# Optimization experiments

Measured on AMD Instinct MI355X. Metric: run time of the kernel, lower is better.

## Reference

```python
import jax, jax.numpy as jnp
import numpy as np
from jax import lax

T, H, K, V, O = 8192, 2048, 512, 512, 2048


def setup_inputs() -> dict:
    key = jax.random.key(0)
    ks = jax.random.split(key, 11)
    s_h = 1.0 / np.sqrt(H)
    s_v = 1.0 / np.sqrt(V)
    return {
        "hidden_state": jax.random.normal(ks[0], (T, H), jnp.float32),
        "Wq": jax.random.normal(ks[1], (H, K), jnp.float32) * s_h,
        "bq": jax.random.normal(ks[2], (K,), jnp.float32) * 0.02,
        "Wk": jax.random.normal(ks[3], (H, K), jnp.float32) * s_h,
        "bk": jax.random.normal(ks[4], (K,), jnp.float32) * 0.02,
        "Wv": jax.random.normal(ks[5], (H, V), jnp.float32) * s_h,
        "bv": jax.random.normal(ks[6], (V,), jnp.float32) * 0.02,
        "Wg": jax.random.normal(ks[7], (H, K), jnp.float32) * s_h,
        "bg": jax.random.normal(ks[8], (K,), jnp.float32) * 0.02,
        "Wo": jax.random.normal(ks[9], (V, O), jnp.float32) * s_v,
        "bo": jax.random.normal(ks[10], (O,), jnp.float32) * 0.02,
    }


def reference(hidden_state, Wq, bq, Wk, bk, Wv, bv, Wg, bg, Wo, bo):
    # Batched projections (torch Linear: x @ W^T + b; here W stored as [in,out])
    q = hidden_state @ Wq + bq                    # [T, K]
    k = jax.nn.sigmoid(hidden_state @ Wk + bk)    # [T, K]
    g = jax.nn.sigmoid(hidden_state @ Wg + bg)    # [T, K]
    v = hidden_state @ Wv + bv                    # [T, V]

    def step(state, qkvg):
        qi, ki, vi, gi = qkvg
        # state: [K, V]; gated decay per key-dim row, then outer-product write
        state = state * gi[:, None] + ki[:, None] * vi[None, :]
        out_i = qi @ state  # == state.T @ qi -> [V]
        return state, out_i

    init = jnp.zeros((K, V), hidden_state.dtype)
    final_state, outs = lax.scan(step, init, (q, k, v, g))  # outs: [T, V]
    output = outs @ Wo + bo                                  # [T, O]
    return output, final_state
```

## Files before the change

kernel.cpp:

```cpp
#include <hip/hip_runtime.h>

#define T_LEN 8192
#define H_DIM 2048
#define K_DIM 512
#define V_DIM 512
#define O_DIM 2048
#define CHUNK 64
#define NCHUNK 128
#define CGROUP 64

typedef short bf16x8 __attribute__((ext_vector_type(8)));
typedef float f32x4 __attribute__((ext_vector_type(4)));

typedef const __attribute__((address_space(1))) void* gptr1_t;
typedef __attribute__((address_space(3))) void* lptr3_t;

__device__ __forceinline__ float b2f(unsigned short u) {
    unsigned int i = ((unsigned int)u) << 16;
    float f;
    __builtin_memcpy(&f, &i, 4);
    return f;
}
__device__ __forceinline__ unsigned short f2b(float f) {
    unsigned int i;
    __builtin_memcpy(&i, &f, 4);
    unsigned int r = (i + 0x7FFFu + ((i >> 16) & 1u)) >> 16;
    return (unsigned short)r;
}
__device__ __forceinline__ float fw(float v) {
    return fminf(fmaxf(v, -1e30f), 1e30f);
}

__global__ __launch_bounds__(256) void conv2bf_k(const float* __restrict__ in,
                                                 unsigned short* __restrict__ out,
                                                 long N) {
    long i = ((long)blockIdx.x * 256 + threadIdx.x) * 8;
    if (i >= N) return;
    unsigned int w[4];
#pragma unroll
    for (int u = 0; u < 4; u++) {
        unsigned short lo = f2b(in[i + 2 * u]);
        unsigned short hi = f2b(in[i + 2 * u + 1]);
        w[u] = (unsigned int)lo | ((unsigned int)hi << 16);
    }
    uint4 pk; pk.x = w[0]; pk.y = w[1]; pk.z = w[2]; pk.w = w[3];
    *(uint4*)(out + i) = pk;
}

__global__ __launch_bounds__(64) void probe_k(int* __restrict__ flag) {
    __shared__ unsigned short As[16 * 32];
    __shared__ unsigned short Bs[16 * 32];
    int tid = threadIdx.x;
    for (int idx = tid; idx < 512; idx += 64) {
        int r = idx >> 5, c = idx & 31;
        float av = (c == 0) ? (float)(r + 1) : (c == 1 ? 1.0f : 0.0f);
        float bv = (c == 0) ? 1.0f : (c == 1 ? (float)(1024 * (r + 1)) : 0.0f);
        As[r * 32 + c] = f2b(av);
        Bs[r * 32 + c] = f2b(bv);
    }
    __syncthreads();
    int ln15 = tid & 15, q4 = (tid & 63) >> 4;
    bf16x8 a = *(const bf16x8*)(As + ln15 * 32 + q4 * 8);
    bf16x8 b = *(const bf16x8*)(Bs + ln15 * 32 + q4 * 8);
    f32x4 acc = {0.f, 0.f, 0.f, 0.f};
    acc = __builtin_amdgcn_mfma_f32_16x16x32_bf16(a, b, acc, 0, 0, 0);
    bool h0 = true, h1 = true;
#pragma unroll
    for (int i = 0; i < 4; i++) {
        float e0 = (float)((q4 * 4 + i + 1) + 1024 * (ln15 + 1));
        float e1 = (float)((ln15 + 1) + 1024 * (q4 * 4 + i + 1));
        h0 = h0 && (acc[i] == e0);
        h1 = h1 && (acc[i] == e1);
    }
    unsigned long long b0 = __ballot(h0 ? 1 : 0);
    unsigned long long b1 = __ballot(h1 ? 1 : 0);
    if (tid == 0) *flag = (b0 == ~0ull) ? 0 : ((b1 == ~0ull) ? 1 : 0);
}

template <int DF>
__global__ __launch_bounds__(256) void transpose_k(const void* __restrict__ in,
                                                   unsigned short* __restrict__ out,
                                                   int R, int C) {
    __shared__ unsigned short tile[32][33];
    int br = blockIdx.x, bc = blockIdx.y;
    int tc = threadIdx.x & 31, tr = threadIdx.x >> 5;
#pragma unroll
    for (int i = 0; i < 4; i++) {
        int r = tr + 8 * i;
        long idx = (long)(br * 32 + r) * C + bc * 32 + tc;
        tile[r][tc] = DF ? f2b(((const float*)in)[idx]) : ((const unsigned short*)in)[idx];
    }
    __syncthreads();
#pragma unroll
    for (int i = 0; i < 4; i++) {
        int r = tr + 8 * i;
        out[(long)(bc * 32 + r) * R + br * 32 + tc] = tile[tc][r];
    }
}

__global__ __launch_bounds__(256) void proj_gemm_k(const unsigned short* __restrict__ A,
                                                   const unsigned short* __restrict__ WT,
                                                   const float* __restrict__ bq,
                                                   const float* __restrict__ bk,
                                                   const float* __restrict__ bg,
                                                   const float* __restrict__ bv,
                                                   unsigned short* __restrict__ qb,
                                                   unsigned short* __restrict__ kb,
                                                   float* __restrict__ gb,
                                                   unsigned short* __restrict__ vT,
                                                   const int* __restrict__ flagp) {
    __shared__ unsigned short As[128 * 32];
    __shared__ unsigned short Bs[128 * 32];
    int fl = *flagp;
    int tid = threadIdx.x;
    int lane = tid & 63;
    int w = tid >> 6;
    int ln15 = lane & 15, q4 = lane >> 4;
    int wm = w >> 1, wn = w & 1;
    long m0 = (long)blockIdx.x * 128, n0 = (long)blockIdx.y * 128;

    f32x4 acc[4][4] = {};

    for (int kt = 0; kt < H_DIM; kt += 32) {
        __syncthreads();
#pragma unroll
        for (int it = 0; it < 2; it++) {
            int chunk = it * 256 + tid;
            int row = chunk >> 2;
            int col = (chunk & 3) * 8;
            const unsigned short* ga = A + (m0 + row) * (long)H_DIM + kt + col;
            const unsigned short* gb_ = WT + (n0 + row) * (long)H_DIM + kt + col;
            __builtin_amdgcn_global_load_lds((gptr1_t)(const void*)ga,
                                             (lptr3_t)(void*)(As + chunk * 8), 16, 0, 0);
            __builtin_amdgcn_global_load_lds((gptr1_t)(const void*)gb_,
                                             (lptr3_t)(void*)(Bs + chunk * 8), 16, 0, 0);
        }
        __syncthreads();
        bf16x8 a[4], b[4];
#pragma unroll
        for (int i = 0; i < 4; i++)
            a[i] = *(const bf16x8*)(As + (wm * 64 + 16 * i + ln15) * 32 + q4 * 8);
#pragma unroll
        for (int j = 0; j < 4; j++)
            b[j] = *(const bf16x8*)(Bs + (wn * 64 + 16 * j + ln15) * 32 + q4 * 8);
#pragma unroll
        for (int i = 0; i < 4; i++)
#pragma unroll
            for (int j = 0; j < 4; j++)
                acc[i][j] = __builtin_amdgcn_mfma_f32_16x16x32_bf16(a[i], b[j], acc[i][j], 0, 0, 0);
    }

    int seg = (int)(n0 >> 9);
    int nl0 = (int)(n0 & 511);
    const float* bias = seg == 0 ? bq : seg == 1 ? bk : seg == 2 ? bg : bv;

    if (seg == 3 && fl == 0) {
#pragma unroll
        for (int i = 0; i < 4; i++)
#pragma unroll
            for (int j = 0; j < 4; j++) {
                int nl = nl0 + wn * 64 + 16 * j + ln15;
                float bsv = bias[nl];
                long mb = m0 + wm * 64 + 16 * i + q4 * 4;
                unsigned short h0 = f2b(fw(acc[i][j][0] + bsv));
                unsigned short h1 = f2b(fw(acc[i][j][1] + bsv));
                unsigned short h2 = f2b(fw(acc[i][j][2] + bsv));
                unsigned short h3 = f2b(fw(acc[i][j][3] + bsv));
                uint2 pk;
                pk.x = (unsigned int)h0 | ((unsigned int)h1 << 16);
                pk.y = (unsigned int)h2 | ((unsigned int)h3 << 16);
                *(uint2*)(vT + (long)nl * T_LEN + mb) = pk;
            }
    } else {
#pragma unroll
        for (int i = 0; i < 4; i++)
#pragma unroll
            for (int j = 0; j < 4; j++)
#pragma unroll
                for (int ii = 0; ii < 4; ii++) {
                    int dm = fl ? ln15 : q4 * 4 + ii;
                    int dn = fl ? q4 * 4 + ii : ln15;
                    long m = m0 + wm * 64 + 16 * i + dm;
                    int nl = nl0 + wn * 64 + 16 * j + dn;
                    float v = fw(acc[i][j][ii] + bias[nl]);
                    if (seg == 1 || seg == 2) v = 1.0f / (1.0f + __expf(-v));
                    if (seg == 0)
                        qb[m * K_DIM + nl] = f2b(v);
                    else if (seg == 1)
                        kb[m * K_DIM + nl] = f2b(v);
                    else if (seg == 2)
                        gb[m * K_DIM + nl] = v;
                    else
                        vT[(long)nl * T_LEN + m] = f2b(v);
                }
    }
}

__global__ __launch_bounds__(256) void gemm_f32_k(const unsigned short* __restrict__ A,
                                                  const unsigned short* __restrict__ BT,
                                                  const float* __restrict__ bias,
                                                  float* __restrict__ out,
                                                  int M, int N, int K,
                                                  const int* __restrict__ flagp) {
    __shared__ unsigned short As[128 * 32];
    __shared__ unsigned short Bs[128 * 32];
    int fl = *flagp;
    int tid = threadIdx.x;
    int lane = tid & 63;
    int w = tid >> 6;
    int ln15 = lane & 15, q4 = lane >> 4;
    int wm = w >> 1, wn = w & 1;
    long m0 = (long)blockIdx.x * 128, n0 = (long)blockIdx.y * 128;

    f32x4 acc[4][4] = {};

    for (int kt = 0; kt < K; kt += 32) {
        __syncthreads();
#pragma unroll
        for (int it = 0; it < 2; it++) {
            int chunk = it * 256 + tid;
            int row = chunk >> 2;
            int col = (chunk & 3) * 8;
            const unsigned short* ga = A + (m0 + row) * (long)K + kt + col;
            const unsigned short* gbp = BT + (n0 + row) * (long)K + kt + col;
            __builtin_amdgcn_global_load_lds((gptr1_t)(const void*)ga,
                                             (lptr3_t)(void*)(As + chunk * 8), 16, 0, 0);
            __builtin_amdgcn_global_load_lds((gptr1_t)(const void*)gbp,
                                             (lptr3_t)(void*)(Bs + chunk * 8), 16, 0, 0);
        }
        __syncthreads();
        bf16x8 a[4], b[4];
#pragma unroll
        for (int i = 0; i < 4; i++)
            a[i] = *(const bf16x8*)(As + (wm * 64 + 16 * i + ln15) * 32 + q4 * 8);
#pragma unroll
        for (int j = 0; j < 4; j++)
            b[j] = *(const bf16x8*)(Bs + (wn * 64 + 16 * j + ln15) * 32 + q4 * 8);
#pragma unroll
        for (int i = 0; i < 4; i++)
#pragma unroll
            for (int j = 0; j < 4; j++)
                acc[i][j] = __builtin_amdgcn_mfma_f32_16x16x32_bf16(a[i], b[j], acc[i][j], 0, 0, 0);
    }

#pragma unroll
    for (int i = 0; i < 4; i++)
#pragma unroll
        for (int j = 0; j < 4; j++)
#pragma unroll
            for (int ii = 0; ii < 4; ii++) {
                int dm = fl ? ln15 : q4 * 4 + ii;
                int dn = fl ? q4 * 4 + ii : ln15;
                long m = m0 + wm * 64 + 16 * i + dm;
                long n = n0 + wn * 64 + 16 * j + dn;
                out[m * N + n] = fw(acc[i][j][ii] + bias[n]);
            }
}

__global__ __launch_bounds__(256) void cumprod_k(const float* __restrict__ g,
                                                 unsigned short* __restrict__ q,
                                                 unsigned short* __restrict__ k,
                                                 unsigned short* __restrict__ khatT,
                                                 float* __restrict__ pend) {
    int c = blockIdx.x;
    int d = blockIdx.y * 256 + threadIdx.x;
    long base = (long)c * CHUNK * K_DIM + d;
    float P = 1.0f;
    for (int s = 0; s < CHUNK; s++) P = fmaxf(P * g[base + (long)s * K_DIM], 1e-37f);
    pend[c * K_DIM + d] = P;
    float Pend = P;
    P = 1.0f;
    for (int s8 = 0; s8 < CHUNK; s8 += 8) {
        unsigned int packed[4];
#pragma unroll
        for (int u = 0; u < 8; u++) {
            int s = s8 + u;
            long idx = base + (long)s * K_DIM;
            P = fmaxf(P * g[idx], 1e-37f);
            float qv = fw(b2f(q[idx]) * P);
            q[idx] = f2b(qv);
            float kv = b2f(k[idx]);
            float kt = kv / P;
            kt = fmaxf(fminf(kt, 3e37f), -3e37f);
            k[idx] = f2b(kt);
            float ratio = Pend / P;
            unsigned short kh = f2b(fw(kv * ratio));
            if (u & 1)
                packed[u >> 1] |= ((unsigned int)kh) << 16;
            else
                packed[u >> 1] = kh;
        }
        uint4 pk;
        pk.x = packed[0]; pk.y = packed[1]; pk.z = packed[2]; pk.w = packed[3];
        *(uint4*)(khatT + (long)d * T_LEN + c * CHUNK + s8) = pk;
    }
}

__global__ __launch_bounds__(256) void scan_k(const unsigned short* __restrict__ khatT,
                                              const unsigned short* __restrict__ vT,
                                              const float* __restrict__ pend,
                                              unsigned short* __restrict__ ST,
                                              float* __restrict__ Sio,
                                              int c0, int cn,
                                              const int* __restrict__ flagp) {
    int fl = *flagp;
    int lane = threadIdx.x & 63, w = threadIdx.x >> 6;
    int ln15 = lane & 15, q4 = lane >> 4;
    int k0 = (blockIdx.x & 15) * 32 + (w & 1) * 16;
    int v0 = (blockIdx.x >> 4) * 32 + (w >> 1) * 16;
    f32x4 acc;
#pragma unroll
    for (int i = 0; i < 4; i++) {
        int dk = fl ? ln15 : q4 * 4 + i;
        int dv = fl ? q4 * 4 + i : ln15;
        acc[i] = Sio[(long)(k0 + dk) * V_DIM + v0 + dv];
    }
    for (int c = c0; c < cn; c++) {
        long cloc = c - c0;
        if (!fl) {
            uint2 pk;
            pk.x = (unsigned int)f2b(fw(acc[0])) | ((unsigned int)f2b(fw(acc[1])) << 16);
            pk.y = (unsigned int)f2b(fw(acc[2])) | ((unsigned int)f2b(fw(acc[3])) << 16);
            *(uint2*)(ST + (cloc * V_DIM + v0 + ln15) * K_DIM + k0 + q4 * 4) = pk;
            float4 pd = *(const float4*)(pend + c * K_DIM + k0 + q4 * 4);
            acc[0] *= pd.x; acc[1] *= pd.y; acc[2] *= pd.z; acc[3] *= pd.w;
        } else {
#pragma unroll
            for (int i = 0; i < 4; i++)
                ST[(cloc * V_DIM + v0 + q4 * 4 + i) * K_DIM + k0 + ln15] = f2b(fw(acc[i]));
            float pd = pend[c * K_DIM + k0 + ln15];
#pragma unroll
            for (int i = 0; i < 4; i++) acc[i] *= pd;
        }
#pragma unroll
        for (int s0 = 0; s0 < CHUNK; s0 += 32) {
            bf16x8 a = *(const bf16x8*)(khatT + (long)(k0 + ln15) * T_LEN + c * CHUNK + s0 + q4 * 8);
            bf16x8 b = *(const bf16x8*)(vT + (long)(v0 + ln15) * T_LEN + c * CHUNK + s0 + q4 * 8);
            acc = __builtin_amdgcn_mfma_f32_16x16x32_bf16(a, b, acc, 0, 0, 0);
        }
    }
#pragma unroll
    for (int i = 0; i < 4; i++) {
        int dk = fl ? ln15 : q4 * 4 + i;
        int dv = fl ? q4 * 4 + i : ln15;
        Sio[(long)(k0 + dk) * V_DIM + v0 + dv] = fw(acc[i]);
    }
}

__global__ __launch_bounds__(256) void copy_state_k(const float* __restrict__ S,
                                                    float* __restrict__ out) {
    long i = (long)blockIdx.x * 1024 + threadIdx.x * 4;
    *(float4*)(out + i) = *(const float4*)(S + i);
}

__global__ __launch_bounds__(256) void intra_k(const unsigned short* __restrict__ qs,
                                               const unsigned short* __restrict__ ks,
                                               const unsigned short* __restrict__ vT,
                                               const unsigned short* __restrict__ ST,
                                               unsigned short* __restrict__ outs,
                                               int c_base,
                                               const int* __restrict__ flagp) {
    __shared__ unsigned short Ab[64 * 72];
    int fl = *flagp;
    long cloc = blockIdx.x >> 1;
    int c = c_base + (int)cloc, h = blockIdx.x & 1;
    int lane = threadIdx.x & 63, w = threadIdx.x >> 6;
    int ln15 = lane & 15, q4 = lane >> 4;
    long t0 = (long)c * CHUNK;

    {
        f32x4 accA[4] = {};
        for (int kk = 0; kk < K_DIM; kk += 32) {
            bf16x8 a = *(const bf16x8*)(qs + (t0 + 16 * w + ln15) * K_DIM + kk + q4 * 8);
#pragma unroll
            for (int j = 0; j < 4; j++) {
                bf16x8 b = *(const bf16x8*)(ks + (t0 + 16 * j + ln15) * K_DIM + kk + q4 * 8);
                accA[j] = __builtin_amdgcn_mfma_f32_16x16x32_bf16(a, b, accA[j], 0, 0, 0);
            }
        }
#pragma unroll
        for (int j = 0; j < 4; j++)
#pragma unroll
            for (int i = 0; i < 4; i++) {
                int dt = fl ? ln15 : q4 * 4 + i;
                int ds = fl ? q4 * 4 + i : ln15;
                int tl = 16 * w + dt;
                int s = 16 * j + ds;
                float av = (s <= tl) ? accA[j][i] : 0.0f;
                Ab[tl * 72 + s] = f2b(fw(av));
            }
    }
    __syncthreads();

    int v0 = h * 256 + w * 64;
    f32x4 acc[4][4] = {};
    for (int kk = 0; kk < K_DIM; kk += 32) {
        bf16x8 a[4], b[4];
#pragma unroll
        for (int i = 0; i < 4; i++)
            a[i] = *(const bf16x8*)(qs + (t0 + 16 * i + ln15) * K_DIM + kk + q4 * 8);
#pragma unroll
        for (int j = 0; j < 4; j++)
            b[j] = *(const bf16x8*)(ST + (cloc * V_DIM + v0 + 16 * j + ln15) * K_DIM + kk + q4 * 8);
#pragma unroll
        for (int i = 0; i < 4; i++)
#pragma unroll
            for (int j = 0; j < 4; j++)
                acc[i][j] = __builtin_amdgcn_mfma_f32_16x16x32_bf16(a[i], b[j], acc[i][j], 0, 0, 0);
    }
#pragma unroll
    for (int s0 = 0; s0 < CHUNK; s0 += 32) {
        bf16x8 a[4], b[4];
#pragma unroll
        for (int i = 0; i < 4; i++)
            a[i] = *(const bf16x8*)(Ab + (16 * i + ln15) * 72 + s0 + q4 * 8);
#pragma unroll
        for (int j = 0; j < 4; j++)
            b[j] = *(const bf16x8*)(vT + (long)(v0 + 16 * j + ln15) * T_LEN + t0 + s0 + q4 * 8);
#pragma unroll
        for (int i = 0; i < 4; i++)
#pragma unroll
            for (int j = 0; j < 4; j++)
                acc[i][j] = __builtin_amdgcn_mfma_f32_16x16x32_bf16(a[i], b[j], acc[i][j], 0, 0, 0);
    }
#pragma unroll
    for (int i = 0; i < 4; i++)
#pragma unroll
        for (int j = 0; j < 4; j++)
#pragma unroll
            for (int ii = 0; ii < 4; ii++) {
                int dt = fl ? ln15 : q4 * 4 + ii;
                int dv = fl ? q4 * 4 + ii : ln15;
                outs[(t0 + 16 * i + dt) * V_DIM + v0 + 16 * j + dv] = f2b(fw(acc[i][j][ii]));
            }
}

extern "C" void kernel_launch(void* const* d_in, const int* in_sizes, int n_in,
                              void* d_out, int out_size, void* d_ws, size_t ws_size,
                              hipStream_t stream) {
    const float* hs = (const float*)d_in[0];
    const float* Wq = (const float*)d_in[1];
    const float* bq = (const float*)d_in[2];
    const float* Wk = (const float*)d_in[3];
    const float* bk = (const float*)d_in[4];
    const float* Wv = (const float*)d_in[5];
    const float* bv = (const float*)d_in[6];
    const float* Wg = (const float*)d_in[7];
    const float* bg = (const float*)d_in[8];
    const float* Wo = (const float*)d_in[9];
    const float* bo = (const float*)d_in[10];

    float* out = (float*)d_out;

    char* ws = (char*)d_ws;
    const size_t MB = 1024 * 1024;
    unsigned short* WT = (unsigned short*)(ws + 0 * MB);
    unsigned short* WoT = (unsigned short*)(ws + 8 * MB);
    unsigned short* qb = (unsigned short*)(ws + 10 * MB);
    unsigned short* kb = (unsigned short*)(ws + 18 * MB);
    unsigned short* vTb = (unsigned short*)(ws + 26 * MB);
    float* gb = (float*)(ws + 34 * MB);
    unsigned short* outsb = (unsigned short*)(ws + 34 * MB);
    unsigned short* khatT = (unsigned short*)(ws + 50 * MB);
    float* pend = (float*)(ws + 58 * MB);
    int* flags = (int*)(ws + 58 * MB + 256 * 1024);
    float* Scarry = (float*)(ws + 59 * MB);
    unsigned short* STb = (unsigned short*)(ws + 60 * MB);
    unsigned short* hsb = (unsigned short*)(ws + 60 * MB);
    float* fsspare = (float*)(ws + 92 * MB);
    (void)ws_size; (void)in_sizes; (void)n_in;

    float* finalst =
        ((long)out_size >= (long)T_LEN * O_DIM + (long)K_DIM * V_DIM)
            ? out + (long)T_LEN * O_DIM
            : fsspare;

    dim3 b256(256);
    hipMemsetAsync(flags, 0, 16, stream);
    probe_k<<<dim3(1), dim3(64), 0, stream>>>(flags);
    conv2bf_k<<<dim3(8192), b256, 0, stream>>>(hs, hsb, (long)T_LEN * H_DIM);
    transpose_k<1><<<dim3(H_DIM / 32, K_DIM / 32), b256, 0, stream>>>(Wq, WT + 0 * 512 * H_DIM, H_DIM, K_DIM);
    transpose_k<1><<<dim3(H_DIM / 32, K_DIM / 32), b256, 0, stream>>>(Wk, WT + 1 * 512 * H_DIM, H_DIM, K_DIM);
    transpose_k<1><<<dim3(H_DIM / 32, K_DIM / 32), b256, 0, stream>>>(Wg, WT + 2 * 512 * H_DIM, H_DIM, K_DIM);
    transpose_k<1><<<dim3(H_DIM / 32, V_DIM / 32), b256, 0, stream>>>(Wv, WT + 3 * 512 * H_DIM, H_DIM, V_DIM);
    transpose_k<1><<<dim3(V_DIM / 32, O_DIM / 32), b256, 0, stream>>>(Wo, WoT, V_DIM, O_DIM);
    proj_gemm_k<<<dim3(T_LEN / 128, 16), b256, 0, stream>>>(
        hsb, WT, bq, bk, bg, bv, qb, kb, gb, vTb, flags);
    cumprod_k<<<dim3(NCHUNK, K_DIM / 256), b256, 0, stream>>>(gb, qb, kb, khatT, pend);
    hipMemsetAsync(Scarry, 0, (size_t)K_DIM * V_DIM * 4, stream);
    scan_k<<<dim3(256), b256, 0, stream>>>(khatT, vTb, pend, STb, Scarry, 0, CGROUP, flags);
    intra_k<<<dim3(2 * CGROUP), b256, 0, stream>>>(qb, kb, vTb, STb, outsb, 0, flags);
    scan_k<<<dim3(256), b256, 0, stream>>>(khatT, vTb, pend, STb, Scarry, CGROUP, NCHUNK, flags);
    intra_k<<<dim3(2 * CGROUP), b256, 0, stream>>>(qb, kb, vTb, STb, outsb, CGROUP, flags);
    copy_state_k<<<dim3((K_DIM * V_DIM) / 1024), b256, 0, stream>>>(Scarry, finalst);
    gemm_f32_k<<<dim3(T_LEN / 128, O_DIM / 128), b256, 0, stream>>>(
        outsb, WoT, bo, out, T_LEN, O_DIM, V_DIM, flags);
}
```

Before: 482.1 us.

## Rewrite projection GEMM as 256x256 tile double-buffered pipelined kernel with swizzled LDS

```diff
diff --git a/kernel.cpp b/kernel.cpp
--- a/kernel.cpp
+++ b/kernel.cpp
@@ -98,56 +98,153 @@
     }
 }
 
-__global__ __launch_bounds__(256) void proj_gemm_k(const unsigned short* __restrict__ A,
-                                                   const unsigned short* __restrict__ WT,
-                                                   const float* __restrict__ bq,
-                                                   const float* __restrict__ bk,
-                                                   const float* __restrict__ bg,
-                                                   const float* __restrict__ bv,
-                                                   unsigned short* __restrict__ qb,
-                                                   unsigned short* __restrict__ kb,
-                                                   float* __restrict__ gb,
-                                                   unsigned short* __restrict__ vT,
-                                                   const int* __restrict__ flagp) {
-    __shared__ unsigned short As[128 * 32];
-    __shared__ unsigned short Bs[128 * 32];
+__global__ __launch_bounds__(512, 2) void proj_gemm256_k(const unsigned short* __restrict__ A,
+                                                         const unsigned short* __restrict__ WT,
+                                                         const float* __restrict__ bq,
+                                                         const float* __restrict__ bk,
+                                                         const float* __restrict__ bg,
+                                                         const float* __restrict__ bv,
+                                                         unsigned short* __restrict__ qb,
+                                                         unsigned short* __restrict__ kb,
+                                                         float* __restrict__ gb,
+                                                         unsigned short* __restrict__ vT,
+                                                         const int* __restrict__ flagp) {
+    __shared__ unsigned short As[2][256 * 64];
+    __shared__ unsigned short Bs[2][256 * 64];
     int fl = *flagp;
     int tid = threadIdx.x;
     int lane = tid & 63;
+    int ln15 = lane & 15, q4 = lane >> 4;
     int w = tid >> 6;
-    int ln15 = lane & 15, q4 = lane >> 4;
-    int wm = w >> 1, wn = w & 1;
-    long m0 = (long)blockIdx.x * 128, n0 = (long)blockIdx.y * 128;
-
-    f32x4 acc[4][4] = {};
-
-    for (int kt = 0; kt < H_DIM; kt += 32) {
-        __syncthreads();
-#pragma unroll
-        for (int it = 0; it < 2; it++) {
-            int chunk = it * 256 + tid;
-            int row = chunk >> 2;
-            int col = (chunk & 3) * 8;
-            const unsigned short* ga = A + (m0 + row) * (long)H_DIM + kt + col;
-            const unsigned short* gb_ = WT + (n0 + row) * (long)H_DIM + kt + col;
-            __builtin_amdgcn_global_load_lds((gptr1_t)(const void*)ga,
-                                             (lptr3_t)(void*)(As + chunk * 8), 16, 0, 0);
-            __builtin_amdgcn_global_load_lds((gptr1_t)(const void*)gb_,
-                                             (lptr3_t)(void*)(Bs + chunk * 8), 16, 0, 0);
-        }
-        __syncthreads();
-        bf16x8 a[4], b[4];
-#pragma unroll
-        for (int i = 0; i < 4; i++)
-            a[i] = *(const bf16x8*)(As + (wm * 64 + 16 * i + ln15) * 32 + q4 * 8);
-#pragma unroll
-        for (int j = 0; j < 4; j++)
-            b[j] = *(const bf16x8*)(Bs + (wn * 64 + 16 * j + ln15) * 32 + q4 * 8);
-#pragma unroll
-        for (int i = 0; i < 4; i++)
-#pragma unroll
-            for (int j = 0; j < 4; j++)
-                acc[i][j] = __builtin_amdgcn_mfma_f32_16x16x32_bf16(a[i], b[j], acc[i][j], 0, 0, 0);
+    int wm = w >> 2, wn = w & 3;
+    long m0 = (long)blockIdx.x * 256, n0 = (long)blockIdx.y * 256;
+
+    int idx0 = tid, idx1 = 512 + tid;
+    int r0_ = idx0 >> 3, r1_ = idx1 >> 3;
+    int c80 = (idx0 & 7) ^ (r0_ & 7);
+    int c81 = (idx1 & 7) ^ (r1_ & 7);
+    int trA0 = ((r0_ >> 6) & 1) * 128 + (r0_ & 63);
+    int trA1 = ((r1_ >> 6) & 1) * 128 + (r1_ & 63);
+    int tcB0 = ((r0_ >> 5) & 3) * 64 + (r0_ & 31);
+    int tcB1 = ((r1_ >> 5) & 3) * 64 + (r1_ & 31);
+    const unsigned short* gA0 = A + (m0 + trA0) * (long)H_DIM + c80 * 8;
+    const unsigned short* gA1 = A + (m0 + trA1) * (long)H_DIM + c81 * 8;
+    const unsigned short* gB0 = WT + (n0 + tcB0) * (long)H_DIM + c80 * 8;
+    const unsigned short* gB1 = WT + (n0 + tcB1) * (long)H_DIM + c81 * 8;
+    int ld0 = idx0 * 8, ld1 = idx1 * 8;
+
+#define STAGE_A(buf, half, ks)                                                              \
+    do {                                                                                    \
+        __builtin_amdgcn_global_load_lds(                                                   \
+            (gptr1_t)(const void*)(gA0 + (long)(half) * 64 * H_DIM + (ks)),                 \
+            (lptr3_t)(void*)(&As[buf][(half) * 8192 + ld0]), 16, 0, 0);                     \
+        __builtin_amdgcn_global_load_lds(                                                   \
+            (gptr1_t)(const void*)(gA1 + (long)(half) * 64 * H_DIM + (ks)),                 \
+            (lptr3_t)(void*)(&As[buf][(half) * 8192 + ld1]), 16, 0, 0);                     \
+    } while (0)
+#define STAGE_B(buf, half, ks)                                                              \
+    do {                                                                                    \
+        __builtin_amdgcn_global_load_lds(                                                   \
+            (gptr1_t)(const void*)(gB0 + (long)(half) * 32 * H_DIM + (ks)),                 \
+            (lptr3_t)(void*)(&Bs[buf][(half) * 8192 + ld0]), 16, 0, 0);                     \
+        __builtin_amdgcn_global_load_lds(                                                   \
+            (gptr1_t)(const void*)(gB1 + (long)(half) * 32 * H_DIM + (ks)),                 \
+            (lptr3_t)(void*)(&Bs[buf][(half) * 8192 + ld1]), 16, 0, 0);                     \
+    } while (0)
+
+    auto LDA = [&](int buf, int im, int s) -> bf16x8 {
+        int row = (im >> 2) * 128 + wm * 64 + (im & 3) * 16 + ln15;
+        int cb = (s * 64 + q4 * 16) ^ ((row & 7) << 4);
+        return *(const bf16x8*)((const unsigned short*)As[buf] + row * 64 + (cb >> 1));
+    };
+    auto LDB = [&](int buf, int jn, int s) -> bf16x8 {
+        int row = (jn >> 1) * 128 + wn * 32 + (jn & 1) * 16 + ln15;
+        int cb = (s * 64 + q4 * 16) ^ ((row & 7) << 4);
+        return *(const bf16x8*)((const unsigned short*)Bs[buf] + row * 64 + (cb >> 1));
+    };
+
+    f32x4 acc[8][4] = {};
+
+    STAGE_A(0, 0, 0);
+    STAGE_B(0, 0, 0);
+    STAGE_B(0, 1, 0);
+    STAGE_A(0, 1, 0);
+    STAGE_A(1, 0, 64);
+    STAGE_B(1, 0, 64);
+    asm volatile("s_waitcnt vmcnt(4)" ::: "memory");
+    __builtin_amdgcn_s_barrier();
+
+    int cur = 0;
+    for (int kt = 0; kt < H_DIM; kt += 64, cur ^= 1) {
+        int k1 = (kt + 64) & (H_DIM - 1);
+        int k2 = (kt + 128) & (H_DIM - 1);
+        bf16x8 af[4][2], blo[2][2], bhi[2][2];
+
+#pragma unroll
+        for (int i = 0; i < 4; i++) { af[i][0] = LDA(cur, i, 0); af[i][1] = LDA(cur, i, 1); }
+#pragma unroll
+        for (int j = 0; j < 2; j++) { blo[j][0] = LDB(cur, j, 0); blo[j][1] = LDB(cur, j, 1); }
+        STAGE_B(cur ^ 1, 1, k1);
+        __builtin_amdgcn_s_barrier();
+        asm volatile("s_waitcnt lgkmcnt(0)" ::: "memory");
+        __builtin_amdgcn_sched_barrier(0);
+        __builtin_amdgcn_s_setprio(1);
+#pragma unroll
+        for (int i = 0; i < 4; i++)
+#pragma unroll
+            for (int j = 0; j < 2; j++) {
+                acc[i][j] = __builtin_amdgcn_mfma_f32_16x16x32_bf16(af[i][0], blo[j][0], acc[i][j], 0, 0, 0);
+                acc[i][j] = __builtin_amdgcn_mfma_f32_16x16x32_bf16(af[i][1], blo[j][1], acc[i][j], 0, 0, 0);
+            }
+        __builtin_amdgcn_s_setprio(0);
+        __builtin_amdgcn_s_barrier();
+
+#pragma unroll
+        for (int j = 0; j < 2; j++) { bhi[j][0] = LDB(cur, 2 + j, 0); bhi[j][1] = LDB(cur, 2 + j, 1); }
+        STAGE_A(cur ^ 1, 1, k1);
+        __builtin_amdgcn_s_barrier();
+        asm volatile("s_waitcnt lgkmcnt(0)" ::: "memory");
+        __builtin_amdgcn_sched_barrier(0);
+        __builtin_amdgcn_s_setprio(1);
+#pragma unroll
+        for (int i = 0; i < 4; i++)
+#pragma unroll
+            for (int j = 0; j < 2; j++) {
+                acc[i][2 + j] = __builtin_amdgcn_mfma_f32_16x16x32_bf16(af[i][0], bhi[j][0], acc[i][2 + j], 0, 0, 0);
+                acc[i][2 + j] = __builtin_amdgcn_mfma_f32_16x16x32_bf16(af[i][1], bhi[j][1], acc[i][2 + j], 0, 0, 0);
+            }
+        __builtin_amdgcn_s_setprio(0);
+        __builtin_amdgcn_s_barrier();
+
+#pragma unroll
+        for (int i = 0; i < 4; i++) { af[i][0] = LDA(cur, 4 + i, 0); af[i][1] = LDA(cur, 4 + i, 1); }
+        STAGE_A(cur, 0, k2);
+        __builtin_amdgcn_s_barrier();
+        asm volatile("s_waitcnt lgkmcnt(0)" ::: "memory");
+        __builtin_amdgcn_sched_barrier(0);
+        __builtin_amdgcn_s_setprio(1);
+#pragma unroll
+        for (int i = 0; i < 4; i++)
+#pragma unroll
+            for (int j = 0; j < 2; j++) {
+                acc[4 + i][2 + j] = __builtin_amdgcn_mfma_f32_16x16x32_bf16(af[i][0], bhi[j][0], acc[4 + i][2 + j], 0, 0, 0);
+                acc[4 + i][2 + j] = __builtin_amdgcn_mfma_f32_16x16x32_bf16(af[i][1], bhi[j][1], acc[4 + i][2 + j], 0, 0, 0);
+            }
+        __builtin_amdgcn_s_setprio(0);
+        __builtin_amdgcn_s_barrier();
+
+        STAGE_B(cur, 0, k2);
+        __builtin_amdgcn_s_setprio(1);
+#pragma unroll
+        for (int i = 0; i < 4; i++)
+#pragma unroll
+            for (int j = 0; j < 2; j++) {
+                acc[4 + i][j] = __builtin_amdgcn_mfma_f32_16x16x32_bf16(af[i][0], blo[j][0], acc[4 + i][j], 0, 0, 0);
+                acc[4 + i][j] = __builtin_amdgcn_mfma_f32_16x16x32_bf16(af[i][1], blo[j][1], acc[4 + i][j], 0, 0, 0);
+            }
+        __builtin_amdgcn_s_setprio(0);
+        asm volatile("s_waitcnt vmcnt(4)" ::: "memory");
+        __builtin_amdgcn_s_barrier();
     }
 
     int seg = (int)(n0 >> 9);
@@ -156,16 +253,16 @@
 
     if (seg == 3 && fl == 0) {
 #pragma unroll
-        for (int i = 0; i < 4; i++)
-#pragma unroll
-            for (int j = 0; j < 4; j++) {
-                int nl = nl0 + wn * 64 + 16 * j + ln15;
+        for (int im = 0; im < 8; im++)
+#pragma unroll
+            for (int jn = 0; jn < 4; jn++) {
+                int nl = nl0 + wn * 64 + (jn >> 1) * 32 + (jn & 1) * 16 + ln15;
                 float bsv = bias[nl];
-                long mb = m0 + wm * 64 + 16 * i + q4 * 4;
-                unsigned short h0 = f2b(fw(acc[i][j][0] + bsv));
-                unsigned short h1 = f2b(fw(acc[i][j][1] + bsv));
-                unsigned short h2 = f2b(fw(acc[i][j][2] + bsv));
-                unsigned short h3 = f2b(fw(acc[i][j][3] + bsv));
+                long mb = m0 + wm * 128 + (im >> 2) * 64 + (im & 3) * 16 + q4 * 4;
+                unsigned short h0 = f2b(fw(acc[im][jn][0] + bsv));
+                unsigned short h1 = f2b(fw(acc[im][jn][1] + bsv));
+                unsigned short h2 = f2b(fw(acc[im][jn][2] + bsv));
+                unsigned short h3 = f2b(fw(acc[im][jn][3] + bsv));
                 uint2 pk;
                 pk.x = (unsigned int)h0 | ((unsigned int)h1 << 16);
                 pk.y = (unsigned int)h2 | ((unsigned int)h3 << 16);
@@ -173,16 +270,16 @@
             }
     } else {
 #pragma unroll
-        for (int i = 0; i < 4; i++)
-#pragma unroll
-            for (int j = 0; j < 4; j++)
+        for (int im = 0; im < 8; im++)
+#pragma unroll
+            for (int jn = 0; jn < 4; jn++)
 #pragma unroll
                 for (int ii = 0; ii < 4; ii++) {
                     int dm = fl ? ln15 : q4 * 4 + ii;
                     int dn = fl ? q4 * 4 + ii : ln15;
-                    long m = m0 + wm * 64 + 16 * i + dm;
-                    int nl = nl0 + wn * 64 + 16 * j + dn;
-                    float v = fw(acc[i][j][ii] + bias[nl]);
+                    long m = m0 + wm * 128 + (im >> 2) * 64 + (im & 3) * 16 + dm;
+                    int nl = nl0 + wn * 64 + (jn >> 1) * 32 + (jn & 1) * 16 + dn;
+                    float v = fw(acc[im][jn][ii] + bias[nl]);
                     if (seg == 1 || seg == 2) v = 1.0f / (1.0f + __expf(-v));
                     if (seg == 0)
                         qb[m * K_DIM + nl] = f2b(v);
@@ -194,6 +291,8 @@
                         vT[(long)nl * T_LEN + m] = f2b(v);
                 }
     }
+#undef STAGE_A
+#undef STAGE_B
 }
 
 __global__ __launch_bounds__(256) void gemm_f32_k(const unsigned short* __restrict__ A,
@@ -484,7 +583,7 @@
     transpose_k<1><<<dim3(H_DIM / 32, K_DIM / 32), b256, 0, stream>>>(Wg, WT + 2 * 512 * H_DIM, H_DIM, K_DIM);
     transpose_k<1><<<dim3(H_DIM / 32, V_DIM / 32), b256, 0, stream>>>(Wv, WT + 3 * 512 * H_DIM, H_DIM, V_DIM);
     transpose_k<1><<<dim3(V_DIM / 32, O_DIM / 32), b256, 0, stream>>>(Wo, WoT, V_DIM, O_DIM);
-    proj_gemm_k<<<dim3(T_LEN / 128, 16), b256, 0, stream>>>(
+    proj_gemm256_k<<<dim3(T_LEN / 256, 8), dim3(512), 0, stream>>>(
         hsb, WT, bq, bk, bg, bv, qb, kb, gb, vTb, flags);
     cumprod_k<<<dim3(NCHUNK, K_DIM / 256), b256, 0, stream>>>(gb, qb, kb, khatT, pend);
     hipMemsetAsync(Scarry, 0, (size_t)K_DIM * V_DIM * 4, stream);
```

Result: faster. 455.7 us (-5.5%).
